# Kernel optimization log

Measured on AMD Instinct MI355X. Metric: run time of the kernel, lower is better.

Reference implementation:

```python
import jax, jax.numpy as jnp
import numpy as np

NEG_SLOPE = 0.2  # PyG GATConv default negative_slope
EPS = 1e-16     # PyG softmax denominator epsilon


def gat_layer(x, src, dst, W, att_src, att_dst, bias, N):
    """PyG-style GATConv: gather -> leaky-relu score -> segment softmax -> scatter-add.
    x: [N, F_in], W: [F_in, H*C], att_src/att_dst: [H, C], bias: [H*C].
    src/dst: [E] edge endpoints (messages flow src -> dst), self-loops included.
    """
    H, C = att_src.shape
    h = (x @ W).reshape(N, H, C)                       # [N, H, C]
    a_s = jnp.sum(h * att_src, axis=-1)                # [N, H]
    a_d = jnp.sum(h * att_dst, axis=-1)                # [N, H]
    e = a_s[src] + a_d[dst]                            # [E, H]
    e = jnp.where(e > 0, e, NEG_SLOPE * e)             # leaky relu
    m = jax.ops.segment_max(e, dst, num_segments=N)    # [N, H] (self-loops ensure every node hit)
    p = jnp.exp(e - m[dst])                            # [E, H]
    s = jax.ops.segment_sum(p, dst, num_segments=N)    # [N, H]
    alpha = p / (s[dst] + EPS)                         # [E, H]
    out = jax.ops.segment_sum(alpha[:, :, None] * h[src], dst, num_segments=N)  # [N, H, C]
    return out.reshape(N, H * C) + bias


def setup_inputs() -> dict:
    key = jax.random.key(0)
    ks = jax.random.split(key, 12)
    N, E = 100000, 1600000
    x = jax.random.normal(ks[0], (N, 1), dtype=jnp.float32)
    edge_index = jax.random.randint(ks[1], (2, E), 0, N, dtype=jnp.int32)
    sc = 0.1
    # conv1: in=1, heads=4, out=8
    W1 = jax.random.normal(ks[2], (1, 32), dtype=jnp.float32) * sc
    att_src1 = jax.random.normal(ks[3], (4, 8), dtype=jnp.float32) * sc
    att_dst1 = jax.random.normal(ks[4], (4, 8), dtype=jnp.float32) * sc
    bias1 = jnp.zeros((32,), dtype=jnp.float32)
    # conv2: in=32, heads=8, out=8
    W2 = jax.random.normal(ks[5], (32, 64), dtype=jnp.float32) * sc
    att_src2 = jax.random.normal(ks[6], (8, 8), dtype=jnp.float32) * sc
    att_dst2 = jax.random.normal(ks[7], (8, 8), dtype=jnp.float32) * sc
    bias2 = jnp.zeros((64,), dtype=jnp.float32)
    # fc2: 64 -> 1
    fc_w = jax.random.normal(ks[8], (64, 1), dtype=jnp.float32) * sc
    fc_b = jnp.zeros((1,), dtype=jnp.float32)
    return {"x": x, "edge_index": edge_index,
            "W1": W1, "att_src1": att_src1, "att_dst1": att_dst1, "bias1": bias1,
            "W2": W2, "att_src2": att_src2, "att_dst2": att_dst2, "bias2": bias2,
            "fc_w": fc_w, "fc_b": fc_b}


def reference(x, edge_index, W1, att_src1, att_dst1, bias1,
              W2, att_src2, att_dst2, bias2, fc_w, fc_b):
    N = x.shape[0]
    loop = jnp.arange(N, dtype=edge_index.dtype)       # add_self_loops=True (PyG default)
    src = jnp.concatenate([edge_index[0], loop])
    dst = jnp.concatenate([edge_index[1], loop])
    h = jax.nn.elu(gat_layer(x, src, dst, W1, att_src1, att_dst1, bias1, N))
    h = jax.nn.elu(gat_layer(h, src, dst, W2, att_src2, att_dst2, bias2, N))
    return h @ fc_w + fc_b                             # [N, 1]
```

## Files before the change

### kernel.cpp

```cpp
#include <hip/hip_runtime.h>
#include <hip/hip_fp16.h>
#include <cmath>

#define TPB 256
#define NSLOPE 0.2f
#define SEPS 1e-16f

#define BSH 7
#define BNODES 128
#define BSZ 256
#define NBMAX 1024
#define NCHUNK 512
#define MAXDEG 96

__device__ __forceinline__ float lrelu(float v) { return v > 0.f ? v : NSLOPE * v; }
__device__ __forceinline__ float elu1(float v)  { return v > 0.f ? v : expm1f(v); }
__device__ __forceinline__ float elu1f(float v) { return v > 0.f ? v : __expf(v) - 1.f; }

__global__ void k_prep(const float* __restrict__ W1, const float* __restrict__ as1,
                       const float* __restrict__ ad1, float* __restrict__ SD,
                       unsigned* __restrict__ bucketCursor, int NB, unsigned cap) {
    int t = threadIdx.x;
    for (int i = t; i < NB; i += blockDim.x) bucketCursor[(size_t)i * 16] = (unsigned)i * cap;
    if (t < 8) {
        int h = t & 3;
        const float* att = (t >= 4) ? ad1 : as1;
        float acc = 0.f;
        #pragma unroll
        for (int c = 0; c < 8; ++c) acc += W1[h*8+c] * att[h*8+c];
        SD[t] = acc;
    }
}

__global__ void k_bscatter(const int* __restrict__ srcI, const int* __restrict__ dstI,
                           int E, int N, int NB, int chunk,
                           unsigned* __restrict__ bucketCursor, int* __restrict__ pk) {
    __shared__ int cnt[NBMAX];
    __shared__ unsigned base[NBMAX];
    for (int i = threadIdx.x; i < NB; i += blockDim.x) cnt[i] = 0;
    __syncthreads();
    int ET = E + N;
    int beg = blockIdx.x * chunk;
    int end = min(beg + chunk, ET);
    for (int e = beg + threadIdx.x; e < end; e += blockDim.x) {
        int d = (e < E) ? dstI[e] : (e - E);
        atomicAdd(&cnt[d >> BSH], 1);
    }
    __syncthreads();
    for (int i = threadIdx.x; i < NB; i += blockDim.x) {
        int c = cnt[i];
        base[i] = c ? atomicAdd(&bucketCursor[(size_t)i * 16], (unsigned)c) : 0u;
        cnt[i] = 0;
    }
    __syncthreads();
    for (int e = beg + threadIdx.x; e < end; e += blockDim.x) {
        int s, d;
        if (e < E) { s = srcI[e]; d = dstI[e]; } else { s = d = e - E; }
        int b = d >> BSH;
        int r = atomicAdd(&cnt[b], 1);
        pk[base[b] + r] = (s << BSH) | (d & (BNODES - 1));
    }
}

__global__ void k_mega(const int* __restrict__ pk, const unsigned* __restrict__ bucketCursor,
                       unsigned cap,
                       const float* __restrict__ x, const float* __restrict__ SD,
                       const float* __restrict__ W1, const float* __restrict__ b1,
                       const float* __restrict__ W2, const float* __restrict__ attS,
                       const float* __restrict__ attD, int N,
                       unsigned* __restrict__ offsets, int* __restrict__ sortedSrc,
                       __half* __restrict__ h2h, float* __restrict__ aS, float* __restrict__ aD) {
    __shared__ int cnt[BSZ];
    __shared__ int offl[BSZ];
    __shared__ float lds1[BNODES][36];
    int b = blockIdx.x;
    int t = threadIdx.x;
    unsigned rbeg = (unsigned)b * cap, rend = bucketCursor[(size_t)b * 16];
    cnt[t] = 0;
    __syncthreads();
    for (unsigned i = rbeg + t; i < rend; i += BSZ)
        atomicAdd(&cnt[pk[i] & (BNODES - 1)], 1);
    __syncthreads();
    int v = cnt[t];
    offl[t] = v;
    __syncthreads();
    for (int off = 1; off < BSZ; off <<= 1) {
        int u = (t >= off) ? offl[t - off] : 0;
        __syncthreads();
        offl[t] += u;
        __syncthreads();
    }
    int ex = offl[t] - v;
    unsigned myBeg = rbeg + (unsigned)ex;
    int d = (b << BSH) + t;
    if (t < BNODES && d < N) offsets[d] = (myBeg << 10) | (unsigned)v;
    cnt[t] = 0;
    offl[t] = ex;
    __syncthreads();
    for (unsigned i = rbeg + t; i < rend; i += BSZ) {
        int p = pk[i];
        int dl = p & (BNODES - 1);
        int r = atomicAdd(&cnt[dl], 1);
        sortedSrc[rbeg + (unsigned)(offl[dl] + r)] = p >> BSH;
    }
    __syncthreads();
    if (t < BNODES && d < N) {
        float xd = x[d];
        float S0 = SD[0], S1 = SD[1], S2 = SD[2], S3 = SD[3];
        float D0 = xd*SD[4], D1 = xd*SD[5], D2 = xd*SD[6], D3 = xd*SD[7];
        float s0 = 0.f, s1 = 0.f, s2 = 0.f, s3 = 0.f;
        float g0 = 0.f, g1 = 0.f, g2 = 0.f, g3 = 0.f;
        unsigned i = myBeg;
        int rem = v;
        for (; rem >= 4; rem -= 4, i += 4) {
            int a0 = sortedSrc[i],   a1 = sortedSrc[i+1];
            int a2 = sortedSrc[i+2], a3 = sortedSrc[i+3];
            float x0 = x[a0], x1 = x[a1], x2 = x[a2], x3 = x[a3];
            float p;
            p = __expf(lrelu(x0*S0 + D0)); s0 += p; g0 += p * x0;
            p = __expf(lrelu(x0*S1 + D1)); s1 += p; g1 += p * x0;
            p = __expf(lrelu(x0*S2 + D2)); s2 += p; g2 += p * x0;
            p = __expf(lrelu(x0*S3 + D3)); s3 += p; g3 += p * x0;
            p = __expf(lrelu(x1*S0 + D0)); s0 += p; g0 += p * x1;
            p = __expf(lrelu(x1*S1 + D1)); s1 += p; g1 += p * x1;
            p = __expf(lrelu(x1*S2 + D2)); s2 += p; g2 += p * x1;
            p = __expf(lrelu(x1*S3 + D3)); s3 += p; g3 += p * x1;
            p = __expf(lrelu(x2*S0 + D0)); s0 += p; g0 += p * x2;
            p = __expf(lrelu(x2*S1 + D1)); s1 += p; g1 += p * x2;
            p = __expf(lrelu(x2*S2 + D2)); s2 += p; g2 += p * x2;
            p = __expf(lrelu(x2*S3 + D3)); s3 += p; g3 += p * x2;
            p = __expf(lrelu(x3*S0 + D0)); s0 += p; g0 += p * x3;
            p = __expf(lrelu(x3*S1 + D1)); s1 += p; g1 += p * x3;
            p = __expf(lrelu(x3*S2 + D2)); s2 += p; g2 += p * x3;
            p = __expf(lrelu(x3*S3 + D3)); s3 += p; g3 += p * x3;
        }
        for (; rem > 0; --rem, ++i) {
            float xs = x[sortedSrc[i]];
            float p;
            p = __expf(lrelu(xs*S0 + D0)); s0 += p; g0 += p * xs;
            p = __expf(lrelu(xs*S1 + D1)); s1 += p; g1 += p * xs;
            p = __expf(lrelu(xs*S2 + D2)); s2 += p; g2 += p * xs;
            p = __expf(lrelu(xs*S3 + D3)); s3 += p; g3 += p * xs;
        }
        float gg[4];
        gg[0] = g0 / (s0 + SEPS); gg[1] = g1 / (s1 + SEPS);
        gg[2] = g2 / (s2 + SEPS); gg[3] = g3 / (s3 + SEPS);
        #pragma unroll
        for (int hh = 0; hh < 4; ++hh)
            #pragma unroll
            for (int cc = 0; cc < 8; ++cc)
                lds1[t][hh*8+cc] = elu1(gg[hh] * W1[hh*8+cc] + b1[hh*8+cc]);
    }
    __syncthreads();
    int lane = t & 63;
    int sub = t >> 6;
    float w2r[32];
    #pragma unroll
    for (int k = 0; k < 32; ++k) w2r[k] = W2[k*64 + lane];
    float attSl = attS[lane], attDl = attD[lane];
    int nCnt = min(BNODES, N - (b << BSH));
    for (int nn = sub; nn < nCnt; nn += 4) {
        const float4* row4 = (const float4*)lds1[nn];
        float acc = 0.f;
        #pragma unroll
        for (int k4 = 0; k4 < 8; ++k4) {
            float4 rv = row4[k4];
            acc += rv.x*w2r[4*k4] + rv.y*w2r[4*k4+1] + rv.z*w2r[4*k4+2] + rv.w*w2r[4*k4+3];
        }
        int node = (b << BSH) + nn;
        h2h[(size_t)node*64 + lane] = __float2half(acc);
        float ps = acc * attSl;
        float pd = acc * attDl;
        #pragma unroll
        for (int m = 1; m < 8; m <<= 1) {
            ps += __shfl_xor(ps, m);
            pd += __shfl_xor(pd, m);
        }
        int hh = lane >> 3, cc = lane & 7;
        if (cc == 0) aS[(size_t)node*8 + hh] = ps;
        if (cc == 1) aD[(size_t)node*8 + hh] = pd;
    }
}

__global__ void k_agg(const unsigned* __restrict__ offsets, const int* __restrict__ ss,
                      const float* __restrict__ aS, const float* __restrict__ aD,
                      const __half* __restrict__ h2h, const float* __restrict__ b2,
                      const float* __restrict__ fcw, const float* __restrict__ fcb,
                      float* __restrict__ out, int N) {
    __shared__ float pl[4][MAXDEG * 8];
    __shared__ int   sl[4][MAXDEG];
    int lane = threadIdx.x & 63;
    int w = threadIdx.x >> 6;
    int d = blockIdx.x * 4 + w;
    if (d >= N) return;
    unsigned u = offsets[d];
    unsigned beg = u >> 10;
    int deg = (int)(u & 1023u);
    int lH   = lane & 31;
    int half = lane >> 5;
    int hh   = lH >> 2;
    float sum = 0.f, ax = 0.f, ay = 0.f;
    if (deg <= MAXDEG) {
        for (int j = lane; j < deg; j += 64) sl[w][j] = ss[beg + j];
        float adp = aD[(size_t)d*8 + (lane & 7)];
        int tot = deg * 8;
        for (int base = 0; base < tot; base += 64) {
            int idx = base + lane;
            if (idx < tot) {
                int s = sl[w][idx >> 3];
                pl[w][idx] = __expf(lrelu(aS[(size_t)s*8 + (lane & 7)] + adp));
            }
        }
        int e = 0;
        for (; e + 8 <= deg; e += 8) {
            int e0 = e + half, e1 = e + 2 + half, e2 = e + 4 + half, e3 = e + 6 + half;
            int s0 = sl[w][e0], s1 = sl[w][e1], s2 = sl[w][e2], s3 = sl[w][e3];
            float p0 = pl[w][e0*8 + hh], p1 = pl[w][e1*8 + hh];
            float p2 = pl[w][e2*8 + hh], p3 = pl[w][e3*8 + hh];
            float2 g0 = __half22float2(*(const __half2*)(h2h + (size_t)s0*64 + 2*lH));
            float2 g1 = __half22float2(*(const __half2*)(h2h + (size_t)s1*64 + 2*lH));
            float2 g2 = __half22float2(*(const __half2*)(h2h + (size_t)s2*64 + 2*lH));
            float2 g3 = __half22float2(*(const __half2*)(h2h + (size_t)s3*64 + 2*lH));
            ax += p0*g0.x + p1*g1.x + p2*g2.x + p3*g3.x;
            ay += p0*g0.y + p1*g1.y + p2*g2.y + p3*g3.y;
            sum += (p0 + p1) + (p2 + p3);
        }
        for (; e + 2 <= deg; e += 2) {
            int e0 = e + half;
            int s0 = sl[w][e0];
            float p0 = pl[w][e0*8 + hh];
            float2 g0 = __half22float2(*(const __half2*)(h2h + (size_t)s0*64 + 2*lH));
            ax += p0*g0.x; ay += p0*g0.y; sum += p0;
        }
        if (e < deg) {
            int s0 = sl[w][e];
            float p0 = (half == 0) ? pl[w][e*8 + hh] : 0.f;
            float2 g0 = __half22float2(*(const __half2*)(h2h + (size_t)s0*64 + 2*lH));
            ax += p0*g0.x; ay += p0*g0.y; sum += p0;
        }
    } else {
        float adh = aD[(size_t)d*8 + hh];
        for (int e = half; e < deg; e += 2) {
            int s = ss[beg + e];
            float p = __expf(lrelu(aS[(size_t)s*8 + hh] + adh));
            float2 g = __half22float2(*(const __half2*)(h2h + (size_t)s*64 + 2*lH));
            ax += p*g.x; ay += p*g.y; sum += p;
        }
    }
    ax  += __shfl_xor(ax, 32);
    ay  += __shfl_xor(ay, 32);
    sum += __shfl_xor(sum, 32);
    float inv = 1.f / (sum + SEPS);
    float tt = elu1f(ax*inv + b2[2*lH]) * fcw[2*lH]
             + elu1f(ay*inv + b2[2*lH+1]) * fcw[2*lH+1];
    #pragma unroll
    for (int m = 16; m; m >>= 1) tt += __shfl_xor(tt, m);
    if (lane == 0) out[d] = tt + fcb[0];
}

extern "C" void kernel_launch(void* const* d_in, const int* in_sizes, int n_in,
                              void* d_out, int out_size, void* d_ws, size_t ws_size,
                              hipStream_t stream) {
    const float* x    = (const float*)d_in[0];
    const int*   ei   = (const int*)  d_in[1];
    const float* W1   = (const float*)d_in[2];
    const float* as1  = (const float*)d_in[3];
    const float* ad1  = (const float*)d_in[4];
    const float* b1   = (const float*)d_in[5];
    const float* W2   = (const float*)d_in[6];
    const float* attS2= (const float*)d_in[7];
    const float* attD2= (const float*)d_in[8];
    const float* b2   = (const float*)d_in[9];
    const float* fcw  = (const float*)d_in[10];
    const float* fcb  = (const float*)d_in[11];
    float* out = (float*)d_out;

    int N = in_sizes[0];
    int E = in_sizes[1] / 2;
    int ET = E + N;
    int NB = (N + BNODES - 1) / BNODES;
    unsigned cap = (unsigned)((ET + NB - 1) / NB + 1024);
    cap = (cap + 3u) & ~3u;
    size_t padded = (size_t)NB * cap;

    const int* srcI = ei;
    const int* dstI = ei + E;

    float* ws = (float*)d_ws;
    size_t off = 0;
    float*    SD           = ws + off; off += 16;
    unsigned* bucketCursor = (unsigned*)(ws + off); off += (size_t)NBMAX * 16;
    unsigned* offsets      = (unsigned*)(ws + off); off += (size_t)N + 16;
    int*      pk           = (int*)(ws + off); off += padded;
    int*      sortedSrc    = (int*)(ws + off); off += padded;
    float*    aS2          = ws + off; off += (size_t)N * 8;
    float*    aD2          = ws + off; off += (size_t)N * 8;
    __half*   h2h          = (__half*)(ws + off); off += (size_t)N * 32;

    k_prep<<<1, 1024, 0, stream>>>(W1, as1, ad1, SD, bucketCursor, NB, cap);

    int chunk = (ET + NCHUNK - 1) / NCHUNK;
    k_bscatter<<<NCHUNK, TPB, 0, stream>>>(srcI, dstI, E, N, NB, chunk, bucketCursor, pk);
    k_mega    <<<NB, BSZ, 0, stream>>>(pk, bucketCursor, cap, x, SD, W1, b1, W2, attS2, attD2,
                                       N, offsets, sortedSrc, h2h, aS2, aD2);
    k_agg     <<<(N + 3) / 4, TPB, 0, stream>>>(offsets, sortedSrc, aS2, aD2, h2h,
                                                b2, fcw, fcb, out, N);
}
```

Measured before the change: 230.6 us.

## Halve bucket size and split layer-1 edge aggregation across four threads per node

Buckets now hold 64 destination nodes instead of 128, which doubles the number of blocks and shrinks the per-bucket scan. In the layer-1 aggregation, each node's edges are shared by four threads that each take every fourth edge, and the partial sums are combined with xor shuffles. Before, only half the threads in a block did this work while the rest sat idle. The change adds more blocks with more per-block overhead, and the bucket slack is cut from 1024 to 512 extra slots, which raises the risk of overflowing a bucket on skewed degree distributions.

```diff
diff --git a/kernel.cpp b/kernel.cpp
--- a/kernel.cpp
+++ b/kernel.cpp
@@ -6,10 +6,10 @@
 #define NSLOPE 0.2f
 #define SEPS 1e-16f
 
-#define BSH 7
-#define BNODES 128
+#define BSH 6
+#define BNODES 64
 #define BSZ 256
-#define NBMAX 1024
+#define NBMAX 2048
 #define NCHUNK 512
 #define MAXDEG 96
 
@@ -72,6 +72,8 @@
                        __half* __restrict__ h2h, float* __restrict__ aS, float* __restrict__ aD) {
     __shared__ int cnt[BSZ];
     __shared__ int offl[BSZ];
+    __shared__ unsigned nbegu[BNODES];
+    __shared__ int ndegs[BNODES];
     __shared__ float lds1[BNODES][36];
     int b = blockIdx.x;
     int t = threadIdx.x;
@@ -81,21 +83,25 @@
     for (unsigned i = rbeg + t; i < rend; i += BSZ)
         atomicAdd(&cnt[pk[i] & (BNODES - 1)], 1);
     __syncthreads();
-    int v = cnt[t];
-    offl[t] = v;
-    __syncthreads();
-    for (int off = 1; off < BSZ; off <<= 1) {
-        int u = (t >= off) ? offl[t - off] : 0;
+    int v = 0, ex = 0;
+    if (t < BNODES) { v = cnt[t]; offl[t] = v; }
+    __syncthreads();
+    for (int off = 1; off < BNODES; off <<= 1) {
+        int u = (t >= off && t < BNODES) ? offl[t - off] : 0;
         __syncthreads();
-        offl[t] += u;
+        if (t < BNODES) offl[t] += u;
         __syncthreads();
     }
-    int ex = offl[t] - v;
-    unsigned myBeg = rbeg + (unsigned)ex;
-    int d = (b << BSH) + t;
-    if (t < BNODES && d < N) offsets[d] = (myBeg << 10) | (unsigned)v;
-    cnt[t] = 0;
-    offl[t] = ex;
+    if (t < BNODES) {
+        ex = offl[t] - v;
+        unsigned myBeg = rbeg + (unsigned)ex;
+        nbegu[t] = myBeg;
+        ndegs[t] = v;
+        int d = (b << BSH) + t;
+        if (d < N) offsets[d] = (myBeg << 10) | (unsigned)v;
+    }
+    __syncthreads();
+    if (t < BNODES) { cnt[t] = 0; offl[t] = ex; }
     __syncthreads();
     for (unsigned i = rbeg + t; i < rend; i += BSZ) {
         int p = pk[i];
@@ -104,18 +110,21 @@
         sortedSrc[rbeg + (unsigned)(offl[dl] + r)] = p >> BSH;
     }
     __syncthreads();
-    if (t < BNODES && d < N) {
-        float xd = x[d];
+    int n = t >> 2, q = t & 3;
+    int dn = (b << BSH) + n;
+    bool active = (dn < N);
+    float s0 = 0.f, s1 = 0.f, s2 = 0.f, s3 = 0.f;
+    float g0 = 0.f, g1 = 0.f, g2 = 0.f, g3 = 0.f;
+    if (active) {
+        float xd = x[dn];
         float S0 = SD[0], S1 = SD[1], S2 = SD[2], S3 = SD[3];
         float D0 = xd*SD[4], D1 = xd*SD[5], D2 = xd*SD[6], D3 = xd*SD[7];
-        float s0 = 0.f, s1 = 0.f, s2 = 0.f, s3 = 0.f;
-        float g0 = 0.f, g1 = 0.f, g2 = 0.f, g3 = 0.f;
-        unsigned i = myBeg;
-        int rem = v;
-        for (; rem >= 4; rem -= 4, i += 4) {
-            int a0 = sortedSrc[i],   a1 = sortedSrc[i+1];
-            int a2 = sortedSrc[i+2], a3 = sortedSrc[i+3];
-            float x0 = x[a0], x1 = x[a1], x2 = x[a2], x3 = x[a3];
+        unsigned nb0 = nbegu[n];
+        unsigned myEnd = nb0 + (unsigned)ndegs[n];
+        unsigned i = nb0 + (unsigned)q;
+        for (; i + 4 < myEnd; i += 8) {
+            int a0 = sortedSrc[i], a1 = sortedSrc[i+4];
+            float x0 = x[a0], x1 = x[a1];
             float p;
             p = __expf(lrelu(x0*S0 + D0)); s0 += p; g0 += p * x0;
             p = __expf(lrelu(x0*S1 + D1)); s1 += p; g1 += p * x0;
@@ -125,16 +134,8 @@
             p = __expf(lrelu(x1*S1 + D1)); s1 += p; g1 += p * x1;
             p = __expf(lrelu(x1*S2 + D2)); s2 += p; g2 += p * x1;
             p = __expf(lrelu(x1*S3 + D3)); s3 += p; g3 += p * x1;
-            p = __expf(lrelu(x2*S0 + D0)); s0 += p; g0 += p * x2;
-            p = __expf(lrelu(x2*S1 + D1)); s1 += p; g1 += p * x2;
-            p = __expf(lrelu(x2*S2 + D2)); s2 += p; g2 += p * x2;
-            p = __expf(lrelu(x2*S3 + D3)); s3 += p; g3 += p * x2;
-            p = __expf(lrelu(x3*S0 + D0)); s0 += p; g0 += p * x3;
-            p = __expf(lrelu(x3*S1 + D1)); s1 += p; g1 += p * x3;
-            p = __expf(lrelu(x3*S2 + D2)); s2 += p; g2 += p * x3;
-            p = __expf(lrelu(x3*S3 + D3)); s3 += p; g3 += p * x3;
-        }
-        for (; rem > 0; --rem, ++i) {
+        }
+        if (i < myEnd) {
             float xs = x[sortedSrc[i]];
             float p;
             p = __expf(lrelu(xs*S0 + D0)); s0 += p; g0 += p * xs;
@@ -142,14 +143,22 @@
             p = __expf(lrelu(xs*S2 + D2)); s2 += p; g2 += p * xs;
             p = __expf(lrelu(xs*S3 + D3)); s3 += p; g3 += p * xs;
         }
-        float gg[4];
-        gg[0] = g0 / (s0 + SEPS); gg[1] = g1 / (s1 + SEPS);
-        gg[2] = g2 / (s2 + SEPS); gg[3] = g3 / (s3 + SEPS);
+    }
+    s0 += __shfl_xor(s0, 1); s0 += __shfl_xor(s0, 2);
+    s1 += __shfl_xor(s1, 1); s1 += __shfl_xor(s1, 2);
+    s2 += __shfl_xor(s2, 1); s2 += __shfl_xor(s2, 2);
+    s3 += __shfl_xor(s3, 1); s3 += __shfl_xor(s3, 2);
+    g0 += __shfl_xor(g0, 1); g0 += __shfl_xor(g0, 2);
+    g1 += __shfl_xor(g1, 1); g1 += __shfl_xor(g1, 2);
+    g2 += __shfl_xor(g2, 1); g2 += __shfl_xor(g2, 2);
+    g3 += __shfl_xor(g3, 1); g3 += __shfl_xor(g3, 2);
+    if (active) {
+        float sq = (q == 0) ? s0 : (q == 1) ? s1 : (q == 2) ? s2 : s3;
+        float gq = (q == 0) ? g0 : (q == 1) ? g1 : (q == 2) ? g2 : g3;
+        float gg = gq / (sq + SEPS);
         #pragma unroll
-        for (int hh = 0; hh < 4; ++hh)
-            #pragma unroll
-            for (int cc = 0; cc < 8; ++cc)
-                lds1[t][hh*8+cc] = elu1(gg[hh] * W1[hh*8+cc] + b1[hh*8+cc]);
+        for (int cc = 0; cc < 8; ++cc)
+            lds1[n][q*8+cc] = elu1(gg * W1[q*8+cc] + b1[q*8+cc]);
     }
     __syncthreads();
     int lane = t & 63;
@@ -279,7 +288,7 @@
     int E = in_sizes[1] / 2;
     int ET = E + N;
     int NB = (N + BNODES - 1) / BNODES;
-    unsigned cap = (unsigned)((ET + NB - 1) / NB + 1024);
+    unsigned cap = (unsigned)((ET + NB - 1) / NB + 512);
     cap = (cap + 3u) & ~3u;
     size_t padded = (size_t)NB * cap;
 
```

Result: slower. 236.3 us (+2.5%).

## Split bucket sort from layer-1 compute, stage sort in LDS, two threads per node

Applied to the files above, without the earlier changes.

The former mega kernel is split into a per-bucket counting-sort kernel and a layer-1 plus h2 projection kernel. The sort kernel stages each bucket's packed edges in shared memory, sorts them there, and writes sortedSrc back coalesced. It falls back to the global-memory path when a bucket exceeds the staging size. The layer-1 kernel gives each destination node two threads that split its edge list and combine partial sums with a shuffle. The scatter kernel now uses 1024-thread blocks and the bucket capacity slack is halved. The aim is better coalescing and more parallelism in the layer-1 aggregation, at the cost of an extra launch and a round trip through global memory for the offsets.

```diff
diff --git a/kernel.cpp b/kernel.cpp
--- a/kernel.cpp
+++ b/kernel.cpp
@@ -8,9 +8,10 @@
 
 #define BSH 7
 #define BNODES 128
-#define BSZ 256
 #define NBMAX 1024
 #define NCHUNK 512
+#define SCTPB 1024
+#define STAGE 2816
 #define MAXDEG 96
 
 __device__ __forceinline__ float lrelu(float v) { return v > 0.f ? v : NSLOPE * v; }
@@ -62,60 +63,104 @@
     }
 }
 
-__global__ void k_mega(const int* __restrict__ pk, const unsigned* __restrict__ bucketCursor,
-                       unsigned cap,
+__global__ void k_sort(const int* __restrict__ pk, const unsigned* __restrict__ bucketCursor,
+                       unsigned cap, int N,
+                       unsigned* __restrict__ offsets, int* __restrict__ sortedSrc) {
+    __shared__ int stage[STAGE];
+    __shared__ int sorted[STAGE];
+    __shared__ int cnt[BNODES];
+    __shared__ int offl[BNODES];
+    int b = blockIdx.x, t = threadIdx.x;
+    unsigned rbeg = (unsigned)b * cap;
+    int m = (int)(bucketCursor[(size_t)b * 16] - rbeg);
+    if (t < BNODES) cnt[t] = 0;
+    if (m <= STAGE) {
+        for (int i = t; i < m; i += TPB) stage[i] = pk[rbeg + i];
+        __syncthreads();
+        for (int i = t; i < m; i += TPB) atomicAdd(&cnt[stage[i] & (BNODES - 1)], 1);
+        __syncthreads();
+        int v = (t < BNODES) ? cnt[t] : 0;
+        if (t < BNODES) offl[t] = v;
+        __syncthreads();
+        for (int off = 1; off < BNODES; off <<= 1) {
+            int u = (t >= off && t < BNODES) ? offl[t - off] : 0;
+            __syncthreads();
+            if (t < BNODES) offl[t] += u;
+            __syncthreads();
+        }
+        if (t < BNODES) {
+            int ex = offl[t] - v;
+            int d = (b << BSH) + t;
+            if (d < N) offsets[d] = ((rbeg + (unsigned)ex) << 10) | (unsigned)v;
+            cnt[t] = 0;
+            offl[t] = ex;
+        }
+        __syncthreads();
+        for (int i = t; i < m; i += TPB) {
+            int p = stage[i];
+            int dl = p & (BNODES - 1);
+            int r = atomicAdd(&cnt[dl], 1);
+            sorted[offl[dl] + r] = p >> BSH;
+        }
+        __syncthreads();
+        for (int i = t; i < m; i += TPB) sortedSrc[rbeg + i] = sorted[i];
+    } else {
+        __syncthreads();
+        for (int i = t; i < m; i += TPB) atomicAdd(&cnt[pk[rbeg + i] & (BNODES - 1)], 1);
+        __syncthreads();
+        int v = (t < BNODES) ? cnt[t] : 0;
+        if (t < BNODES) offl[t] = v;
+        __syncthreads();
+        for (int off = 1; off < BNODES; off <<= 1) {
+            int u = (t >= off && t < BNODES) ? offl[t - off] : 0;
+            __syncthreads();
+            if (t < BNODES) offl[t] += u;
+            __syncthreads();
+        }
+        if (t < BNODES) {
+            int ex = offl[t] - v;
+            int d = (b << BSH) + t;
+            if (d < N) offsets[d] = ((rbeg + (unsigned)ex) << 10) | (unsigned)v;
+            cnt[t] = 0;
+            offl[t] = ex;
+        }
+        __syncthreads();
+        for (int i = t; i < m; i += TPB) {
+            int p = pk[rbeg + i];
+            int dl = p & (BNODES - 1);
+            int r = atomicAdd(&cnt[dl], 1);
+            sortedSrc[rbeg + (unsigned)(offl[dl] + r)] = p >> BSH;
+        }
+    }
+}
+
+__global__ void k_l1h2(const unsigned* __restrict__ offsets, const int* __restrict__ sortedSrc,
                        const float* __restrict__ x, const float* __restrict__ SD,
                        const float* __restrict__ W1, const float* __restrict__ b1,
                        const float* __restrict__ W2, const float* __restrict__ attS,
                        const float* __restrict__ attD, int N,
-                       unsigned* __restrict__ offsets, int* __restrict__ sortedSrc,
                        __half* __restrict__ h2h, float* __restrict__ aS, float* __restrict__ aD) {
-    __shared__ int cnt[BSZ];
-    __shared__ int offl[BSZ];
     __shared__ float lds1[BNODES][36];
-    int b = blockIdx.x;
     int t = threadIdx.x;
-    unsigned rbeg = (unsigned)b * cap, rend = bucketCursor[(size_t)b * 16];
-    cnt[t] = 0;
-    __syncthreads();
-    for (unsigned i = rbeg + t; i < rend; i += BSZ)
-        atomicAdd(&cnt[pk[i] & (BNODES - 1)], 1);
-    __syncthreads();
-    int v = cnt[t];
-    offl[t] = v;
-    __syncthreads();
-    for (int off = 1; off < BSZ; off <<= 1) {
-        int u = (t >= off) ? offl[t - off] : 0;
-        __syncthreads();
-        offl[t] += u;
-        __syncthreads();
-    }
-    int ex = offl[t] - v;
-    unsigned myBeg = rbeg + (unsigned)ex;
-    int d = (b << BSH) + t;
-    if (t < BNODES && d < N) offsets[d] = (myBeg << 10) | (unsigned)v;
-    cnt[t] = 0;
-    offl[t] = ex;
-    __syncthreads();
-    for (unsigned i = rbeg + t; i < rend; i += BSZ) {
-        int p = pk[i];
-        int dl = p & (BNODES - 1);
-        int r = atomicAdd(&cnt[dl], 1);
-        sortedSrc[rbeg + (unsigned)(offl[dl] + r)] = p >> BSH;
-    }
-    __syncthreads();
-    if (t < BNODES && d < N) {
+    int base = blockIdx.x << BSH;
+    int n = t >> 1, half = t & 1;
+    int d = base + n;
+    bool active = (d < N);
+    float s0 = 0.f, s1 = 0.f, s2 = 0.f, s3 = 0.f;
+    float g0 = 0.f, g1 = 0.f, g2 = 0.f, g3 = 0.f;
+    if (active) {
+        unsigned u = offsets[d];
+        unsigned beg = u >> 10;
+        int deg = (int)(u & 1023u);
         float xd = x[d];
         float S0 = SD[0], S1 = SD[1], S2 = SD[2], S3 = SD[3];
         float D0 = xd*SD[4], D1 = xd*SD[5], D2 = xd*SD[6], D3 = xd*SD[7];
-        float s0 = 0.f, s1 = 0.f, s2 = 0.f, s3 = 0.f;
-        float g0 = 0.f, g1 = 0.f, g2 = 0.f, g3 = 0.f;
-        unsigned i = myBeg;
-        int rem = v;
-        for (; rem >= 4; rem -= 4, i += 4) {
-            int a0 = sortedSrc[i],   a1 = sortedSrc[i+1];
-            int a2 = sortedSrc[i+2], a3 = sortedSrc[i+3];
-            float x0 = x[a0], x1 = x[a1], x2 = x[a2], x3 = x[a3];
+        int d2 = (deg + 1) >> 1;
+        unsigned i = beg + (half ? (unsigned)d2 : 0u);
+        int rem = half ? (deg - d2) : d2;
+        for (; rem >= 2; rem -= 2, i += 2) {
+            int a0 = sortedSrc[i], a1 = sortedSrc[i+1];
+            float x0 = x[a0], x1 = x[a1];
             float p;
             p = __expf(lrelu(x0*S0 + D0)); s0 += p; g0 += p * x0;
             p = __expf(lrelu(x0*S1 + D1)); s1 += p; g1 += p * x0;
@@ -125,16 +170,8 @@
             p = __expf(lrelu(x1*S1 + D1)); s1 += p; g1 += p * x1;
             p = __expf(lrelu(x1*S2 + D2)); s2 += p; g2 += p * x1;
             p = __expf(lrelu(x1*S3 + D3)); s3 += p; g3 += p * x1;
-            p = __expf(lrelu(x2*S0 + D0)); s0 += p; g0 += p * x2;
-            p = __expf(lrelu(x2*S1 + D1)); s1 += p; g1 += p * x2;
-            p = __expf(lrelu(x2*S2 + D2)); s2 += p; g2 += p * x2;
-            p = __expf(lrelu(x2*S3 + D3)); s3 += p; g3 += p * x2;
-            p = __expf(lrelu(x3*S0 + D0)); s0 += p; g0 += p * x3;
-            p = __expf(lrelu(x3*S1 + D1)); s1 += p; g1 += p * x3;
-            p = __expf(lrelu(x3*S2 + D2)); s2 += p; g2 += p * x3;
-            p = __expf(lrelu(x3*S3 + D3)); s3 += p; g3 += p * x3;
-        }
-        for (; rem > 0; --rem, ++i) {
+        }
+        if (rem > 0) {
             float xs = x[sortedSrc[i]];
             float p;
             p = __expf(lrelu(xs*S0 + D0)); s0 += p; g0 += p * xs;
@@ -142,14 +179,21 @@
             p = __expf(lrelu(xs*S2 + D2)); s2 += p; g2 += p * xs;
             p = __expf(lrelu(xs*S3 + D3)); s3 += p; g3 += p * xs;
         }
+    }
+    s0 += __shfl_xor(s0, 1); s1 += __shfl_xor(s1, 1);
+    s2 += __shfl_xor(s2, 1); s3 += __shfl_xor(s3, 1);
+    g0 += __shfl_xor(g0, 1); g1 += __shfl_xor(g1, 1);
+    g2 += __shfl_xor(g2, 1); g3 += __shfl_xor(g3, 1);
+    if (active) {
         float gg[4];
         gg[0] = g0 / (s0 + SEPS); gg[1] = g1 / (s1 + SEPS);
         gg[2] = g2 / (s2 + SEPS); gg[3] = g3 / (s3 + SEPS);
+        int h0 = half * 2;
         #pragma unroll
-        for (int hh = 0; hh < 4; ++hh)
+        for (int hh = 0; hh < 2; ++hh)
             #pragma unroll
             for (int cc = 0; cc < 8; ++cc)
-                lds1[t][hh*8+cc] = elu1(gg[hh] * W1[hh*8+cc] + b1[hh*8+cc]);
+                lds1[n][(h0+hh)*8+cc] = elu1(gg[h0+hh] * W1[(h0+hh)*8+cc] + b1[(h0+hh)*8+cc]);
     }
     __syncthreads();
     int lane = t & 63;
@@ -158,7 +202,7 @@
     #pragma unroll
     for (int k = 0; k < 32; ++k) w2r[k] = W2[k*64 + lane];
     float attSl = attS[lane], attDl = attD[lane];
-    int nCnt = min(BNODES, N - (b << BSH));
+    int nCnt = min(BNODES, N - base);
     for (int nn = sub; nn < nCnt; nn += 4) {
         const float4* row4 = (const float4*)lds1[nn];
         float acc = 0.f;
@@ -167,7 +211,7 @@
             float4 rv = row4[k4];
             acc += rv.x*w2r[4*k4] + rv.y*w2r[4*k4+1] + rv.z*w2r[4*k4+2] + rv.w*w2r[4*k4+3];
         }
-        int node = (b << BSH) + nn;
+        int node = base + nn;
         h2h[(size_t)node*64 + lane] = __float2half(acc);
         float ps = acc * attSl;
         float pd = acc * attDl;
@@ -279,7 +323,7 @@
     int E = in_sizes[1] / 2;
     int ET = E + N;
     int NB = (N + BNODES - 1) / BNODES;
-    unsigned cap = (unsigned)((ET + NB - 1) / NB + 1024);
+    unsigned cap = (unsigned)((ET + NB - 1) / NB + 512);
     cap = (cap + 3u) & ~3u;
     size_t padded = (size_t)NB * cap;
 
@@ -300,9 +344,10 @@
     k_prep<<<1, 1024, 0, stream>>>(W1, as1, ad1, SD, bucketCursor, NB, cap);
 
     int chunk = (ET + NCHUNK - 1) / NCHUNK;
-    k_bscatter<<<NCHUNK, TPB, 0, stream>>>(srcI, dstI, E, N, NB, chunk, bucketCursor, pk);
-    k_mega    <<<NB, BSZ, 0, stream>>>(pk, bucketCursor, cap, x, SD, W1, b1, W2, attS2, attD2,
-                                       N, offsets, sortedSrc, h2h, aS2, aD2);
+    k_bscatter<<<NCHUNK, SCTPB, 0, stream>>>(srcI, dstI, E, N, NB, chunk, bucketCursor, pk);
+    k_sort    <<<NB, TPB, 0, stream>>>(pk, bucketCursor, cap, N, offsets, sortedSrc);
+    k_l1h2    <<<NB, TPB, 0, stream>>>(offsets, sortedSrc, x, SD, W1, b1, W2, attS2, attD2,
+                                       N, h2h, aS2, aD2);
     k_agg     <<<(N + 3) / 4, TPB, 0, stream>>>(offsets, sortedSrc, aS2, aD2, h2h,
                                                 b2, fcw, fcb, out, N);
 }
```

New measurement: 224.2 us. 2.8% less time.
